# Optimization experiments

Hardware: AMD Instinct MI355X
Metric: run time of the kernel (lower is better)

## Reference

```python
import jax, jax.numpy as jnp
import numpy as np

N, F, E, H, C, K = 20000, 256, 400000, 4, 64, 3
NEG_SLOPE = 0.2


def setup_inputs() -> dict:
    key = jax.random.key(0)
    ks = jax.random.split(key, 13)
    x = jax.random.normal(ks[0], (N, F), jnp.float32)
    edge0 = jax.random.randint(ks[1], (2, E), 0, N)
    edge1 = jax.random.randint(ks[2], (2, E), 0, N)
    edge2 = jax.random.randint(ks[3], (2, E), 0, N)
    s = 1.0 / np.sqrt(F)
    Wl = jax.random.normal(ks[4], (F, H * C), jnp.float32) * s
    bl = jax.random.normal(ks[5], (H * C,), jnp.float32) * 0.02
    Wr = jax.random.normal(ks[6], (F, H * C), jnp.float32) * s
    br = jax.random.normal(ks[7], (H * C,), jnp.float32) * 0.02
    att = jax.random.normal(ks[8], (K, H, C), jnp.float32) * (1.0 / np.sqrt(C))
    bias_out = jax.random.normal(ks[9], (K, C), jnp.float32) * 0.02
    Wg = jax.random.normal(ks[10], (F, K), jnp.float32) * s
    bg = jax.random.normal(ks[11], (K,), jnp.float32) * 0.02
    return dict(x=x, edge0=edge0, edge1=edge1, edge2=edge2, Wl=Wl, bl=bl,
                Wr=Wr, br=br, att=att, bias_out=bias_out, Wg=Wg, bg=bg)


def _gatv2_hop(xl, xr, src, dst, att_h, b_h, num_nodes):
    # xl, xr: [N, H, C] projected features (shared across hops)
    # att_h: [H, C] hop-specific attention vector; b_h: [C] hop-specific bias
    e = jax.nn.leaky_relu(xl[src] + xr[dst], NEG_SLOPE)          # [E, H, C]
    s = jnp.einsum('ehc,hc->eh', e, att_h)                       # [E, H]
    smax = jax.ops.segment_max(s, dst, num_segments=num_nodes)   # [N, H]
    ex = jnp.exp(s - smax[dst])
    denom = jax.ops.segment_sum(ex, dst, num_segments=num_nodes)
    alpha = ex / denom[dst]                                      # softmax over in-edges of dst
    msg = jax.ops.segment_sum(alpha[:, :, None] * xl[src], dst, num_segments=num_nodes)  # [N,H,C]
    return msg.mean(axis=1) + b_h                                # concat=False -> mean heads


def reference(x, edge0, edge1, edge2, Wl, bl, Wr, br, att, bias_out, Wg, bg):
    num_nodes = x.shape[0]
    heads, ch = att.shape[1], att.shape[2]
    xl = (x @ Wl + bl).reshape(num_nodes, heads, ch)
    xr = (x @ Wr + br).reshape(num_nodes, heads, ch)
    # hop 0: add self-loops (add_self_loops=True only for k == 0)
    loop = jnp.arange(num_nodes, dtype=edge0.dtype)
    src0 = jnp.concatenate([edge0[0], loop])
    dst0 = jnp.concatenate([edge0[1], loop])
    msgs = [
        _gatv2_hop(xl, xr, src0, dst0, att[0], bias_out[0], num_nodes),
        _gatv2_hop(xl, xr, edge1[0], edge1[1], att[1], bias_out[1], num_nodes),
        _gatv2_hop(xl, xr, edge2[0], edge2[1], att[2], bias_out[2], num_nodes),
    ]
    messages = jnp.stack(msgs, axis=1)                 # [N, K, C]
    logits = x @ Wg + bg                               # [N, K]
    weights = jax.nn.softmax(logits, axis=-1)
    return (messages * weights[:, :, None]).sum(axis=1)  # [N, C]
```

## Files before the change

kernel.cpp:

```cpp
#include <hip/hip_runtime.h>
#include <hip/hip_fp16.h>

#define N_NODES 20000
#define FDIM    256
#define NE      400000
#define NK      3
#define LOG2E   1.44269504088896340736f

#define TOT_EDGES (3 * NE + N_NODES)
#define NSEG      (3 * N_NODES)
#define NCHUNK    ((NSEG + 1023) / 1024)

typedef __attribute__((ext_vector_type(8))) _Float16 half8;
typedef __attribute__((ext_vector_type(4))) float f32x4;

#define PK(op, d, a, b) \
    asm("v_pk_" op "_f16 %0, %1, %2" : "=v"(d) : "v"(a), "v"(b))
#define MIX_FH(c, s, w, sel) \
    asm("v_fma_mix_f32 %0, %1, %2, %0 op_sel:[0," sel ",0] op_sel_hi:[0,1,0]" \
        : "+v"(c) : "v"(s), "v"(w))
#define MIX_HH(p, a, b, sel) \
    asm("v_fma_mix_f32 %0, %1, %2, %0 op_sel:[" sel "," sel ",0] op_sel_hi:[1,1,0]" \
        : "+v"(p) : "v"(a), "v"(b))

#define EXP2_ASM(ee, p) \
    asm("s_nop 1\n\t" \
        "v_exp_f32 %0, %1\n\t" \
        "s_nop 3" \
        : "=v"(ee) : "v"(p))

__device__ __forceinline__ float wave_sum(float x)
{
    int v = __float_as_int(x);
    int t;
    t = __builtin_amdgcn_update_dpp(0, v, 0x111, 0xf, 0xf, false);
    v = __float_as_int(__int_as_float(v) + __int_as_float(t));
    t = __builtin_amdgcn_update_dpp(0, v, 0x112, 0xf, 0xf, false);
    v = __float_as_int(__int_as_float(v) + __int_as_float(t));
    t = __builtin_amdgcn_update_dpp(0, v, 0x114, 0xf, 0xf, false);
    v = __float_as_int(__int_as_float(v) + __int_as_float(t));
    t = __builtin_amdgcn_update_dpp(0, v, 0x118, 0xf, 0xf, false);
    v = __float_as_int(__int_as_float(v) + __int_as_float(t));
    t = __builtin_amdgcn_update_dpp(0, v, 0x142, 0xa, 0xf, false);
    v = __float_as_int(__int_as_float(v) + __int_as_float(t));
    t = __builtin_amdgcn_update_dpp(0, v, 0x143, 0xc, 0xf, false);
    v = __float_as_int(__int_as_float(v) + __int_as_float(t));
    return __int_as_float(__builtin_amdgcn_readlane(v, 63));
}

__device__ __forceinline__ float rowsum16(float x)
{
    int v = __float_as_int(x);
    int t;
    t = __builtin_amdgcn_update_dpp(0, v, 0x121, 0xf, 0xf, false);
    v = __float_as_int(__int_as_float(v) + __int_as_float(t));
    t = __builtin_amdgcn_update_dpp(0, v, 0x122, 0xf, 0xf, false);
    v = __float_as_int(__int_as_float(v) + __int_as_float(t));
    t = __builtin_amdgcn_update_dpp(0, v, 0x124, 0xf, 0xf, false);
    v = __float_as_int(__int_as_float(v) + __int_as_float(t));
    t = __builtin_amdgcn_update_dpp(0, v, 0x128, 0xf, 0xf, false);
    v = __float_as_int(__int_as_float(v) + __int_as_float(t));
    return __int_as_float(v);
}

__device__ __forceinline__ void decode_edge(int i, const int* e0, const int* e1,
                                            const int* e2, int& k, int& src,
                                            int& dst)
{
    if (i < NE) {
        k = 0; src = e0[i]; dst = e0[NE + i];
    } else if (i < NE + N_NODES) {
        k = 0; src = i - NE; dst = src;
    } else if (i < 2 * NE + N_NODES) {
        int j = i - (NE + N_NODES);
        k = 1; src = e1[j]; dst = e1[NE + j];
    } else {
        int j = i - (2 * NE + N_NODES);
        k = 2; src = e2[j]; dst = e2[NE + j];
    }
}

#define XCONV_V4 (N_NODES * FDIM / 4)
#define WCONV_T  (512 * 64)
#define ATT_N    (3 * 256)
#define CONV_T   (XCONV_V4 + WCONV_T + ATT_N)
#define CONV_B   ((CONV_T + 255) / 256)
#define EDGE_B   ((TOT_EDGES + 255) / 256)

__global__ __launch_bounds__(256) void prep_kernel(
    const float* __restrict__ x, const float* __restrict__ Wl,
    const float* __restrict__ Wr, const float* __restrict__ att,
    const float* __restrict__ Wg, const float* __restrict__ bg,
    const int* __restrict__ e0, const int* __restrict__ e1,
    const int* __restrict__ e2,
    __half* __restrict__ x16, __half* __restrict__ WT16,
    __half* __restrict__ att16, float* __restrict__ gate,
    int* __restrict__ cnt)
{
    if (blockIdx.x < CONV_B) {
        int tid = blockIdx.x * 256 + threadIdx.x;
        if (tid < XCONV_V4) {
            float4 v = ((const float4*)x)[tid];
            ((__half2*)x16)[tid * 2 + 0] = __floats2half2_rn(v.x, v.y);
            ((__half2*)x16)[tid * 2 + 1] = __floats2half2_rn(v.z, v.w);
            const int lane = threadIdx.x & 63;
            const int n    = tid >> 6;
            const int f0   = lane << 2;
            float p0 = 0.f, p1 = 0.f, p2 = 0.f;
            const float* xe = &v.x;
#pragma unroll
            for (int j = 0; j < 4; ++j) {
                float xj = xe[j];
                p0 = fmaf(xj, Wg[(f0 + j) * 3 + 0], p0);
                p1 = fmaf(xj, Wg[(f0 + j) * 3 + 1], p1);
                p2 = fmaf(xj, Wg[(f0 + j) * 3 + 2], p2);
            }
            p0 = wave_sum(p0); p1 = wave_sum(p1); p2 = wave_sum(p2);
            if (lane == 0) {
                float g0 = exp2f((p0 + bg[0]) * LOG2E);
                float g1 = exp2f((p1 + bg[1]) * LOG2E);
                float g2 = exp2f((p2 + bg[2]) * LOG2E);
                float inv = 1.f / (g0 + g1 + g2);
                gate[n * 3 + 0] = g0 * inv;
                gate[n * 3 + 1] = g1 * inv;
                gate[n * 3 + 2] = g2 * inv;
            }
        } else if (tid < XCONV_V4 + WCONV_T) {
            int q  = tid - XCONV_V4;
            int n  = q & 511;
            int k4 = (q >> 9) << 2;
            const float* Ws = (n < 256) ? Wl : Wr;
            int nn = n & 255;
            float a = Ws[(k4 + 0) * 256 + nn];
            float b = Ws[(k4 + 1) * 256 + nn];
            float c = Ws[(k4 + 2) * 256 + nn];
            float d = Ws[(k4 + 3) * 256 + nn];
            __half2* dst = (__half2*)(WT16 + (size_t)n * 256 + k4);
            dst[0] = __floats2half2_rn(a, b);
            dst[1] = __floats2half2_rn(c, d);
        } else if (tid < CONV_T) {
            int q = tid - XCONV_V4 - WCONV_T;
            att16[q] = __float2half(att[q] * LOG2E);
        }
    } else {
        int i = (blockIdx.x - CONV_B) * 256 + threadIdx.x;
        if (i < TOT_EDGES) {
            int k, src, dst;
            decode_edge(i, e0, e1, e2, k, src, dst);
            atomicAdd(&cnt[k * N_NODES + dst], 1);
        }
    }
}

__global__ __launch_bounds__(256) void gemm_mfma(
    const __half* __restrict__ x16,
    const __half* __restrict__ WT16,
    const float* __restrict__ bl, const float* __restrict__ br,
    __half* __restrict__ XL16, __half* __restrict__ XR16)
{
    __shared__ ushort As[8192];
    __shared__ ushort Bs[8192];
    char* AsB = (char*)As;
    char* BsB = (char*)Bs;

    const int t    = threadIdx.x;
    const int lane = t & 63;
    const int wid  = t >> 6;
    const int wr   = wid >> 1;
    const int wc   = wid & 1;
    const int row0 = blockIdx.x * 128;
    const int col0 = blockIdx.y * 128;
    const int sr   = t >> 1;

    f32x4 acc[4][4] = {};

    for (int k0 = 0; k0 < FDIM; k0 += 64) {
        {
            const __half* src = x16 + (size_t)(row0 + sr) * 256 + k0 + (t & 1) * 32;
            bool ok = (row0 + sr) < N_NODES;
#pragma unroll
            for (int i = 0; i < 4; ++i) {
                uint4 g = ok ? *(const uint4*)(src + i * 8)
                             : make_uint4(0, 0, 0, 0);
                *(uint4*)(AsB + sr * 128 + (((t & 1) * 4 + i) ^ (sr & 7)) * 16) = g;
            }
        }
        {
            const __half* src = WT16 + (size_t)(col0 + sr) * 256 + k0 + (t & 1) * 32;
#pragma unroll
            for (int i = 0; i < 4; ++i) {
                uint4 g = *(const uint4*)(src + i * 8);
                *(uint4*)(BsB + sr * 128 + (((t & 1) * 4 + i) ^ (sr & 7)) * 16) = g;
            }
        }
        __syncthreads();

#pragma unroll
        for (int ks = 0; ks < 2; ++ks) {
            half8 av[4], bv[4];
#pragma unroll
            for (int mi = 0; mi < 4; ++mi) {
                int arow = wr * 64 + mi * 16 + (lane & 15);
                av[mi] = *(const half8*)(AsB + arow * 128 +
                                         (((ks * 4) + (lane >> 4)) ^ (arow & 7)) * 16);
            }
#pragma unroll
            for (int ni = 0; ni < 4; ++ni) {
                int brow = wc * 64 + ni * 16 + (lane & 15);
                bv[ni] = *(const half8*)(BsB + brow * 128 +
                                         (((ks * 4) + (lane >> 4)) ^ (brow & 7)) * 16);
            }
#pragma unroll
            for (int mi = 0; mi < 4; ++mi)
#pragma unroll
                for (int ni = 0; ni < 4; ++ni)
                    acc[mi][ni] = __builtin_amdgcn_mfma_f32_16x16x32_f16(
                        av[mi], bv[ni], acc[mi][ni], 0, 0, 0);
        }
        __syncthreads();
    }

    const bool left   = (col0 < 256);
    __half* dst       = left ? XL16 : XR16;
    const float* bias = left ? bl : br;
    const int cbase   = left ? col0 : (col0 - 256);

#pragma unroll
    for (int mi = 0; mi < 4; ++mi) {
#pragma unroll
        for (int ni = 0; ni < 4; ++ni) {
            int gc = cbase + wc * 64 + ni * 16 + (lane & 15);
            float bv = bias[gc];
#pragma unroll
            for (int i = 0; i < 4; ++i) {
                int rr = row0 + wr * 64 + mi * 16 + (lane >> 4) * 4 + i;
                if (rr < N_NODES)
                    dst[(size_t)rr * 256 + gc] = __float2half(acc[mi][ni][i] + bv);
            }
        }
    }
}

__global__ __launch_bounds__(1024) void scan_pass1(const int* __restrict__ cnt,
                                                   int* __restrict__ bsum)
{
    int i = blockIdx.x * 1024 + threadIdx.x;
    int v = (i < NSEG) ? cnt[i] : 0;
#pragma unroll
    for (int s = 32; s >= 1; s >>= 1) v += __shfl_xor(v, s);
    if ((threadIdx.x & 63) == 0) atomicAdd(&bsum[blockIdx.x], v);
}

__global__ __launch_bounds__(1024) void scan_pass3(const int* __restrict__ cnt,
                                                   const int* __restrict__ bsum,
                                                   int* __restrict__ goff,
                                                   int* __restrict__ cursor)
{
    __shared__ int wsum[16];
    __shared__ int s_boff;
    const int lane = threadIdx.x & 63;
    const int wid  = threadIdx.x >> 6;
    if (wid == 0) {
        int b = (lane < (int)blockIdx.x && lane < NCHUNK) ? bsum[lane] : 0;
#pragma unroll
        for (int s = 32; s >= 1; s >>= 1) b += __shfl_xor(b, s);
        if (lane == 0) s_boff = b;
    }
    int i  = blockIdx.x * 1024 + threadIdx.x;
    int v0 = (i < NSEG) ? cnt[i] : 0;
    int v  = v0;
#pragma unroll
    for (int s = 1; s < 64; s <<= 1) {
        int t = __shfl_up(v, s);
        if (lane >= s) v += t;
    }
    if (lane == 63) wsum[wid] = v;
    __syncthreads();
    if (wid == 0) {
        int ws = (lane < 16) ? wsum[lane] : 0;
#pragma unroll
        for (int s = 1; s < 16; s <<= 1) {
            int t = __shfl_up(ws, s);
            if (lane >= s) ws += t;
        }
        if (lane < 16) wsum[lane] = ws;
    }
    __syncthreads();
    int excl = s_boff + ((wid > 0) ? wsum[wid - 1] : 0) + (v - v0);
    if (i < NSEG) {
        goff[i]   = excl;
        cursor[i] = excl;
        if (i == NSEG - 1) goff[NSEG] = excl + v0;
    }
}

__global__ void scatter_kernel(const int* __restrict__ e0,
                               const int* __restrict__ e1,
                               const int* __restrict__ e2,
                               int* __restrict__ cursor,
                               int* __restrict__ srcs)
{
    for (int i = blockIdx.x * blockDim.x + threadIdx.x; i < TOT_EDGES;
         i += gridDim.x * blockDim.x) {
        int k, src, dst;
        decode_edge(i, e0, e1, e2, k, src, dst);
        int pos = atomicAdd(&cursor[k * N_NODES + dst], 1);
        srcs[pos] = src;
    }
}

__global__ __launch_bounds__(256) void hop_kernel(
    const __half* __restrict__ XL16,
    const __half* __restrict__ XR16,
    const int* __restrict__ goff,
    const int* __restrict__ srcs,
    const __half* __restrict__ att16,
    float* __restrict__ msg)
{
    const int w    = (blockIdx.x * blockDim.x + threadIdx.x) >> 6;
    const int lane = threadIdx.x & 63;
    if (w >= NSEG) return;
    const int k = w / N_NODES;
    const int n = w - k * N_NODES;
    const int lof = lane << 2;

    const uint2 xr = *(const uint2*)(XR16 + ((size_t)n << 8) + lof);
    const uint2 at = *(const uint2*)(att16 + (k << 8) + lof);
    const unsigned K02 = 0x32663266u;

    const int jb  = goff[w];
    const int je  = goff[w + 1];
    const int cnt = je - jb;

    float den = 0.f, c0 = 0.f, c1 = 0.f, c2 = 0.f, c3 = 0.f;

    if (cnt > 0) {
        const int je1 = je - 1;
        int sv = srcs[min(jb + lane, je1)];
        uint2 w0, w1, w2, w3;
        {
            int s_;
            s_ = __builtin_amdgcn_readlane(sv, 0);
            w0 = *(const uint2*)(XL16 + ((size_t)s_ << 8) + lof);
            s_ = __builtin_amdgcn_readlane(sv, min(1, cnt - 1));
            w1 = *(const uint2*)(XL16 + ((size_t)s_ << 8) + lof);
            s_ = __builtin_amdgcn_readlane(sv, min(2, cnt - 1));
            w2 = *(const uint2*)(XL16 + ((size_t)s_ << 8) + lof);
            s_ = __builtin_amdgcn_readlane(sv, min(3, cnt - 1));
            w3 = *(const uint2*)(XL16 + ((size_t)s_ << 8) + lof);
        }

#define EDGE_MATH(W)                                                          \
        {                                                                     \
            unsigned z01, z23, t01, t23, e01, e23;                            \
            PK("add", z01, W.x, xr.x);                                        \
            PK("add", z23, W.y, xr.y);                                        \
            PK("mul", t01, z01, K02);                                         \
            PK("mul", t23, z23, K02);                                         \
            PK("max", e01, z01, t01);                                         \
            PK("max", e23, z23, t23);                                         \
            float p = 0.f;                                                    \
            MIX_HH(p, e01, at.x, "0");                                        \
            MIX_HH(p, e01, at.x, "1");                                        \
            MIX_HH(p, e23, at.y, "0");                                        \
            MIX_HH(p, e23, at.y, "1");                                        \
            p = rowsum16(p);                                                  \
            float ee;                                                         \
            EXP2_ASM(ee, p);                                                  \
            den += ee;                                                        \
            MIX_FH(c0, ee, W.x, "0");                                         \
            MIX_FH(c1, ee, W.x, "1");                                         \
            MIX_FH(c2, ee, W.y, "0");                                         \
            MIX_FH(c3, ee, W.y, "1");                                         \
        }

#define STEP(W, PF) {                                                         \
        EDGE_MATH(W)                                                          \
        if (((PF) & 63) == 0 && (PF) < cnt)                                   \
            sv = srcs[min(jb + (PF) + lane, je1)];                            \
        int s_ = __builtin_amdgcn_readlane(sv, (PF) & 63);                    \
        W = *(const uint2*)(XL16 + ((size_t)s_ << 8) + lof); }

        const int cnt4 = cnt & ~3;
        for (int u = 0; u < cnt4; u += 4) {
            STEP(w0, u + 4);
            STEP(w1, u + 5);
            STEP(w2, u + 6);
            STEP(w3, u + 7);
        }
        const int rem = cnt - cnt4;
        if (rem > 0) EDGE_MATH(w0)
        if (rem > 1) EDGE_MATH(w1)
        if (rem > 2) EDGE_MATH(w2)
#undef STEP
#undef EDGE_MATH
    }

    const float inv = (cnt > 0) ? (0.25f / den) : 0.f;
    float r0 = c0 * inv, r1 = c1 * inv, r2 = c2 * inv, r3 = c3 * inv;
    r0 += __shfl_xor(r0, 16); r0 += __shfl_xor(r0, 32);
    r1 += __shfl_xor(r1, 16); r1 += __shfl_xor(r1, 32);
    r2 += __shfl_xor(r2, 16); r2 += __shfl_xor(r2, 32);
    r3 += __shfl_xor(r3, 16); r3 += __shfl_xor(r3, 32);

    if (lane < 16) {
        float4 r = make_float4(r0, r1, r2, r3);
        *(float4*)(msg + ((size_t)w << 6) + (lane << 2)) = r;
    }
}

__global__ __launch_bounds__(256) void combine_kernel(
    const float* __restrict__ gate, const float* __restrict__ msg,
    const float* __restrict__ bias_out, float* __restrict__ out)
{
    const int n  = blockIdx.x * 16 + (threadIdx.x >> 4);
    const int c4 = (threadIdx.x & 15) << 2;
    if (n >= N_NODES) return;

    float4 o = make_float4(0.f, 0.f, 0.f, 0.f);
#pragma unroll
    for (int k = 0; k < NK; ++k) {
        float g = gate[n * 3 + k];
        float4 m = *(const float4*)(msg +
                     (((size_t)k * N_NODES + n) << 6) + c4);
        float4 b = *(const float4*)(bias_out + (k << 6) + c4);
        o.x = fmaf(g, m.x + b.x, o.x);
        o.y = fmaf(g, m.y + b.y, o.y);
        o.z = fmaf(g, m.z + b.z, o.z);
        o.w = fmaf(g, m.w + b.w, o.w);
    }
    *(float4*)(out + ((size_t)n << 6) + c4) = o;
}

extern "C" void kernel_launch(void* const* d_in, const int* in_sizes, int n_in,
                              void* d_out, int out_size, void* d_ws,
                              size_t ws_size, hipStream_t stream)
{
    const float* x        = (const float*)d_in[0];
    const int*   e0       = (const int*)d_in[1];
    const int*   e1       = (const int*)d_in[2];
    const int*   e2       = (const int*)d_in[3];
    const float* Wl       = (const float*)d_in[4];
    const float* bl       = (const float*)d_in[5];
    const float* Wr       = (const float*)d_in[6];
    const float* br       = (const float*)d_in[7];
    const float* att      = (const float*)d_in[8];
    const float* bias_out = (const float*)d_in[9];
    const float* Wg       = (const float*)d_in[10];
    const float* bg       = (const float*)d_in[11];
    float* out = (float*)d_out;

    char* wsb = (char*)d_ws;
    size_t o = 0;
    __half* x16   = (__half*)(wsb + o); o += (size_t)N_NODES * 256 * sizeof(__half);
    __half* WT16  = (__half*)(wsb + o); o += (size_t)512 * 256 * sizeof(__half);
    __half* att16 = (__half*)(wsb + o); o += (size_t)ATT_N * sizeof(__half);
    __half* XL16  = (__half*)(wsb + o); o += (size_t)N_NODES * 256 * sizeof(__half);
    __half* XR16  = (__half*)(wsb + o); o += (size_t)N_NODES * 256 * sizeof(__half);
    float*  msg   = (float*)(wsb + o);  o += (size_t)NSEG * 64 * sizeof(float);
    int* cnt    = (int*)(wsb + o);   o += (size_t)NSEG * sizeof(int);
    int* bsum   = (int*)(wsb + o);   o += 64 * sizeof(int);
    int* goff   = (int*)(wsb + o);   o += (size_t)(NSEG + 1) * sizeof(int);
    int* cursor = (int*)(wsb + o);   o += (size_t)NSEG * sizeof(int);
    int* srcs   = (int*)(wsb + o);   o += (size_t)TOT_EDGES * sizeof(int);
    float* gate = (float*)(wsb + o); o += (size_t)N_NODES * 3 * sizeof(float);

    hipMemsetAsync(cnt, 0, ((size_t)NSEG + 64) * sizeof(int), stream);

    prep_kernel<<<CONV_B + EDGE_B, 256, 0, stream>>>(
        x, Wl, Wr, att, Wg, bg, e0, e1, e2, x16, WT16, att16, gate, cnt);

    dim3 ggrid((N_NODES + 127) / 128, 4);
    gemm_mfma<<<ggrid, 256, 0, stream>>>(x16, WT16, bl, br, XL16, XR16);

    scan_pass1<<<NCHUNK, 1024, 0, stream>>>(cnt, bsum);
    scan_pass3<<<NCHUNK, 1024, 0, stream>>>(cnt, bsum, goff, cursor);

    int eblocks = (TOT_EDGES + 255) / 256;
    scatter_kernel<<<eblocks, 256, 0, stream>>>(e0, e1, e2, cursor, srcs);

    hop_kernel<<<(NSEG * 64 + 255) / 256, 256, 0, stream>>>(
        XL16, XR16, goff, srcs, att16, msg);

    combine_kernel<<<(N_NODES + 15) / 16, 256, 0, stream>>>(
        gate, msg, bias_out, out);
}
```

Measured before the change: 234.5 us.

## Fuse three hop passes and gated combine into one per-node kernel

The per-(hop,node) attention kernel and the separate combine kernel are merged into one kernel where each wavefront handles a node and loops over all three hops. It accumulates the gate-weighted messages plus bias in registers and writes the output directly. This drops the intermediate msg buffer round trip, one kernel launch, and repeated loads of the XR row. In exchange the grid is three times smaller with longer per-wave serial work, which lowers available parallelism and latency hiding for the gather loads.

```diff
diff --git a/kernel.cpp b/kernel.cpp
--- a/kernel.cpp
+++ b/kernel.cpp
@@ -309,127 +309,117 @@
     }
 }
 
-__global__ __launch_bounds__(256) void hop_kernel(
+__global__ __launch_bounds__(256) void hop3_kernel(
     const __half* __restrict__ XL16,
     const __half* __restrict__ XR16,
     const int* __restrict__ goff,
     const int* __restrict__ srcs,
     const __half* __restrict__ att16,
-    float* __restrict__ msg)
-{
-    const int w    = (blockIdx.x * blockDim.x + threadIdx.x) >> 6;
+    const float* __restrict__ gate,
+    const float* __restrict__ bias_out,
+    float* __restrict__ out)
+{
+    const int n    = (blockIdx.x * blockDim.x + threadIdx.x) >> 6;
     const int lane = threadIdx.x & 63;
-    if (w >= NSEG) return;
-    const int k = w / N_NODES;
-    const int n = w - k * N_NODES;
+    if (n >= N_NODES) return;
     const int lof = lane << 2;
+    const int m4  = (lane & 15) << 2;
 
     const uint2 xr = *(const uint2*)(XR16 + ((size_t)n << 8) + lof);
-    const uint2 at = *(const uint2*)(att16 + (k << 8) + lof);
     const unsigned K02 = 0x32663266u;
 
-    const int jb  = goff[w];
-    const int je  = goff[w + 1];
-    const int cnt = je - jb;
-
-    float den = 0.f, c0 = 0.f, c1 = 0.f, c2 = 0.f, c3 = 0.f;
-
-    if (cnt > 0) {
-        const int je1 = je - 1;
-        int sv = srcs[min(jb + lane, je1)];
-        uint2 w0, w1, w2, w3;
-        {
-            int s_;
-            s_ = __builtin_amdgcn_readlane(sv, 0);
-            w0 = *(const uint2*)(XL16 + ((size_t)s_ << 8) + lof);
-            s_ = __builtin_amdgcn_readlane(sv, min(1, cnt - 1));
-            w1 = *(const uint2*)(XL16 + ((size_t)s_ << 8) + lof);
-            s_ = __builtin_amdgcn_readlane(sv, min(2, cnt - 1));
-            w2 = *(const uint2*)(XL16 + ((size_t)s_ << 8) + lof);
-            s_ = __builtin_amdgcn_readlane(sv, min(3, cnt - 1));
-            w3 = *(const uint2*)(XL16 + ((size_t)s_ << 8) + lof);
-        }
+    float o0 = 0.f, o1 = 0.f, o2 = 0.f, o3 = 0.f;
+
+#pragma unroll
+    for (int k = 0; k < NK; ++k) {
+        const uint2 at = *(const uint2*)(att16 + (k << 8) + lof);
+        const int jb  = goff[k * N_NODES + n];
+        const int je  = goff[k * N_NODES + n + 1];
+        const int cnt = je - jb;
+
+        float den = 0.f, c0 = 0.f, c1 = 0.f, c2 = 0.f, c3 = 0.f;
+
+        if (cnt > 0) {
+            const int je1 = je - 1;
+            int sv = srcs[min(jb + lane, je1)];
+            uint2 w0, w1, w2, w3;
+            {
+                int s_;
+                s_ = __builtin_amdgcn_readlane(sv, 0);
+                w0 = *(const uint2*)(XL16 + ((size_t)s_ << 8) + lof);
+                s_ = __builtin_amdgcn_readlane(sv, min(1, cnt - 1));
+                w1 = *(const uint2*)(XL16 + ((size_t)s_ << 8) + lof);
+                s_ = __builtin_amdgcn_readlane(sv, min(2, cnt - 1));
+                w2 = *(const uint2*)(XL16 + ((size_t)s_ << 8) + lof);
+                s_ = __builtin_amdgcn_readlane(sv, min(3, cnt - 1));
+                w3 = *(const uint2*)(XL16 + ((size_t)s_ << 8) + lof);
+            }
 
 #define EDGE_MATH(W)                                                          \
-        {                                                                     \
-            unsigned z01, z23, t01, t23, e01, e23;                            \
-            PK("add", z01, W.x, xr.x);                                        \
-            PK("add", z23, W.y, xr.y);                                        \
-            PK("mul", t01, z01, K02);                                         \
-            PK("mul", t23, z23, K02);                                         \
-            PK("max", e01, z01, t01);                                         \
-            PK("max", e23, z23, t23);                                         \
-            float p = 0.f;                                                    \
-            MIX_HH(p, e01, at.x, "0");                                        \
-            MIX_HH(p, e01, at.x, "1");                                        \
-            MIX_HH(p, e23, at.y, "0");                                        \
-            MIX_HH(p, e23, at.y, "1");                                        \
-            p = rowsum16(p);                                                  \
-            float ee;                                                         \
-            EXP2_ASM(ee, p);                                                  \
-            den += ee;                                                        \
-            MIX_FH(c0, ee, W.x, "0");                                         \
-            MIX_FH(c1, ee, W.x, "1");                                         \
-            MIX_FH(c2, ee, W.y, "0");                                         \
-            MIX_FH(c3, ee, W.y, "1");                                         \
-        }
+            {                                                                 \
+                unsigned z01, z23, t01, t23, e01, e23;                        \
+                PK("add", z01, W.x, xr.x);                                    \
+                PK("add", z23, W.y, xr.y);                                    \
+                PK("mul", t01, z01, K02);                                     \
+                PK("mul", t23, z23, K02);                                     \
+                PK("max", e01, z01, t01);                                     \
+                PK("max", e23, z23, t23);                                     \
+                float p = 0.f;                                                \
+                MIX_HH(p, e01, at.x, "0");                                    \
+                MIX_HH(p, e01, at.x, "1");                                    \
+                MIX_HH(p, e23, at.y, "0");                                    \
+                MIX_HH(p, e23, at.y, "1");                                    \
+                p = rowsum16(p);                                              \
+                float ee;                                                     \
+                EXP2_ASM(ee, p);                                              \
+                den += ee;                                                    \
+                MIX_FH(c0, ee, W.x, "0");                                     \
+                MIX_FH(c1, ee, W.x, "1");                                     \
+                MIX_FH(c2, ee, W.y, "0");                                     \
+                MIX_FH(c3, ee, W.y, "1");                                     \
+            }
 
 #define STEP(W, PF) {                                                         \
-        EDGE_MATH(W)                                                          \
-        if (((PF) & 63) == 0 && (PF) < cnt)                                   \
-            sv = srcs[min(jb + (PF) + lane, je1)];                            \
-        int s_ = __builtin_amdgcn_readlane(sv, (PF) & 63);                    \
-        W = *(const uint2*)(XL16 + ((size_t)s_ << 8) + lof); }
-
-        const int cnt4 = cnt & ~3;
-        for (int u = 0; u < cnt4; u += 4) {
-            STEP(w0, u + 4);
-            STEP(w1, u + 5);
-            STEP(w2, u + 6);
-            STEP(w3, u + 7);
-        }
-        const int rem = cnt - cnt4;
-        if (rem > 0) EDGE_MATH(w0)
-        if (rem > 1) EDGE_MATH(w1)
-        if (rem > 2) EDGE_MATH(w2)
+            EDGE_MATH(W)                                                      \
+            if (((PF) & 63) == 0 && (PF) < cnt)                               \
+                sv = srcs[min(jb + (PF) + lane, je1)];                        \
+            int s_ = __builtin_amdgcn_readlane(sv, (PF) & 63);                \
+            W = *(const uint2*)(XL16 + ((size_t)s_ << 8) + lof); }
+
+            const int cnt4 = cnt & ~3;
+            for (int u = 0; u < cnt4; u += 4) {
+                STEP(w0, u + 4);
+                STEP(w1, u + 5);
+                STEP(w2, u + 6);
+                STEP(w3, u + 7);
+            }
+            const int rem = cnt - cnt4;
+            if (rem > 0) EDGE_MATH(w0)
+            if (rem > 1) EDGE_MATH(w1)
+            if (rem > 2) EDGE_MATH(w2)
 #undef STEP
 #undef EDGE_MATH
-    }
-
-    const float inv = (cnt > 0) ? (0.25f / den) : 0.f;
-    float r0 = c0 * inv, r1 = c1 * inv, r2 = c2 * inv, r3 = c3 * inv;
-    r0 += __shfl_xor(r0, 16); r0 += __shfl_xor(r0, 32);
-    r1 += __shfl_xor(r1, 16); r1 += __shfl_xor(r1, 32);
-    r2 += __shfl_xor(r2, 16); r2 += __shfl_xor(r2, 32);
-    r3 += __shfl_xor(r3, 16); r3 += __shfl_xor(r3, 32);
+        }
+
+        const float inv = (cnt > 0) ? (0.25f / den) : 0.f;
+        float r0 = c0 * inv, r1 = c1 * inv, r2 = c2 * inv, r3 = c3 * inv;
+        r0 += __shfl_xor(r0, 16); r0 += __shfl_xor(r0, 32);
+        r1 += __shfl_xor(r1, 16); r1 += __shfl_xor(r1, 32);
+        r2 += __shfl_xor(r2, 16); r2 += __shfl_xor(r2, 32);
+        r3 += __shfl_xor(r3, 16); r3 += __shfl_xor(r3, 32);
+
+        const float g  = gate[n * 3 + k];
+        const float4 b = *(const float4*)(bias_out + (k << 6) + m4);
+        o0 = fmaf(g, r0 + b.x, o0);
+        o1 = fmaf(g, r1 + b.y, o1);
+        o2 = fmaf(g, r2 + b.z, o2);
+        o3 = fmaf(g, r3 + b.w, o3);
+    }
 
     if (lane < 16) {
-        float4 r = make_float4(r0, r1, r2, r3);
-        *(float4*)(msg + ((size_t)w << 6) + (lane << 2)) = r;
-    }
-}
-
-__global__ __launch_bounds__(256) void combine_kernel(
-    const float* __restrict__ gate, const float* __restrict__ msg,
-    const float* __restrict__ bias_out, float* __restrict__ out)
-{
-    const int n  = blockIdx.x * 16 + (threadIdx.x >> 4);
-    const int c4 = (threadIdx.x & 15) << 2;
-    if (n >= N_NODES) return;
-
-    float4 o = make_float4(0.f, 0.f, 0.f, 0.f);
-#pragma unroll
-    for (int k = 0; k < NK; ++k) {
-        float g = gate[n * 3 + k];
-        float4 m = *(const float4*)(msg +
-                     (((size_t)k * N_NODES + n) << 6) + c4);
-        float4 b = *(const float4*)(bias_out + (k << 6) + c4);
-        o.x = fmaf(g, m.x + b.x, o.x);
-        o.y = fmaf(g, m.y + b.y, o.y);
-        o.z = fmaf(g, m.z + b.z, o.z);
-        o.w = fmaf(g, m.w + b.w, o.w);
-    }
-    *(float4*)(out + ((size_t)n << 6) + c4) = o;
+        float4 r = make_float4(o0, o1, o2, o3);
+        *(float4*)(out + ((size_t)n << 6) + m4) = r;
+    }
 }
 
 extern "C" void kernel_launch(void* const* d_in, const int* in_sizes, int n_in,
@@ -457,7 +447,6 @@
     __half* att16 = (__half*)(wsb + o); o += (size_t)ATT_N * sizeof(__half);
     __half* XL16  = (__half*)(wsb + o); o += (size_t)N_NODES * 256 * sizeof(__half);
     __half* XR16  = (__half*)(wsb + o); o += (size_t)N_NODES * 256 * sizeof(__half);
-    float*  msg   = (float*)(wsb + o);  o += (size_t)NSEG * 64 * sizeof(float);
     int* cnt    = (int*)(wsb + o);   o += (size_t)NSEG * sizeof(int);
     int* bsum   = (int*)(wsb + o);   o += 64 * sizeof(int);
     int* goff   = (int*)(wsb + o);   o += (size_t)(NSEG + 1) * sizeof(int);
@@ -479,9 +468,6 @@
     int eblocks = (TOT_EDGES + 255) / 256;
     scatter_kernel<<<eblocks, 256, 0, stream>>>(e0, e1, e2, cursor, srcs);
 
-    hop_kernel<<<(NSEG * 64 + 255) / 256, 256, 0, stream>>>(
-        XL16, XR16, goff, srcs, att16, msg);
-
-    combine_kernel<<<(N_NODES + 15) / 16, 256, 0, stream>>>(
-        gate, msg, bias_out, out);
-}
+    hop3_kernel<<<(N_NODES * 64 + 255) / 256, 256, 0, stream>>>(
+        XL16, XR16, goff, srcs, att16, gate, bias_out, out);
+}
```

After: 249.9 us. 6.6% more time.
